# Kernel optimization log

Hardware: AMD Instinct MI355X
Metric: run time of the kernel (lower is better)

The kernel has to match this reference:

```python
import jax, jax.numpy as jnp
import numpy as np

SPARSE_SHAPE = (41, 1600, 1408)  # (D, H, W), batch_size = 1
N_VOXELS = 200000
BN_EPS = 1e-3


def _kernel_offsets():
    # 27 offsets of a 3x3x3 kernel, padding=1 -> offsets in {-1,0,1}^3
    g = np.stack(np.meshgrid(*([np.arange(-1, 2)] * 3), indexing='ij'), axis=-1)
    return jnp.asarray(g.reshape(-1, 3), dtype=jnp.int32)  # (27, 3)


def _neighbor_map(coords):
    """Submanifold rulebook: for each active voxel and each of 27 offsets,
    index of the active neighbor voxel, or N (sentinel) if inactive/out-of-bounds."""
    D, H, W = SPARSE_SHAPE
    N = coords.shape[0]
    b, z, y, x = coords[:, 0], coords[:, 1], coords[:, 2], coords[:, 3]
    flat = ((b * D + z) * H + y) * W + x  # batch_size=1
    grid = jnp.full((D * H * W,), N, dtype=jnp.int32).at[flat].set(
        jnp.arange(N, dtype=jnp.int32))
    offs = _kernel_offsets()                      # (27, 3)
    nc = coords[:, None, 1:4] + offs[None]        # (N, 27, 3)
    lim = jnp.asarray([D, H, W], dtype=jnp.int32)
    valid = jnp.all((nc >= 0) & (nc < lim), axis=-1)  # (N, 27)
    nflat = ((b[:, None] * D + nc[..., 0]) * H + nc[..., 1]) * W + nc[..., 2]
    nbr = jnp.where(valid, grid[jnp.where(valid, nflat, 0)], N)
    return nbr  # (N, 27) int32, sentinel = N


def _subm_conv(features, nbr, w):
    # gather -> batched small GEMM -> (implicit) scatter back to same voxels
    pad = jnp.concatenate(
        [features, jnp.zeros((1, features.shape[1]), features.dtype)], axis=0)
    gathered = pad[nbr]                           # (N, 27, Cin)
    return jnp.einsum('nkc,kcd->nd', gathered, w)  # (N, Cout)


def _bn_relu(x, gamma, beta):
    # BatchNorm1d in train mode over the voxel (batch) dim, eps=1e-3
    mean = x.mean(axis=0)
    var = x.var(axis=0)
    return jax.nn.relu((x - mean) * jax.lax.rsqrt(var + BN_EPS) * gamma + beta)


def setup_inputs() -> dict:
    D, H, W = SPARSE_SHAPE
    total = D * H * W
    rng = np.random.default_rng(0)
    # unique active voxel locations
    flat = np.unique(rng.integers(0, total, size=N_VOXELS + 20000))
    rng.shuffle(flat)
    flat = flat[:N_VOXELS]
    assert flat.shape[0] == N_VOXELS
    z = flat // (H * W)
    y = (flat // W) % H
    x = flat % W
    b = np.zeros_like(z)
    coords = jnp.asarray(np.stack([b, z, y, x], axis=1), dtype=jnp.int32)

    key = jax.random.key(0)
    k0, k1, k2 = jax.random.split(key, 3)
    features = jax.random.uniform(k0, (N_VOXELS, 3), dtype=jnp.float32)
    w1 = jax.random.normal(k1, (27, 3, 16), dtype=jnp.float32) * 0.1
    w2 = jax.random.normal(k2, (27, 16, 16), dtype=jnp.float32) * 0.05
    return {
        'features': features, 'coords': coords,
        'w1': w1, 'gamma1': jnp.ones(16, jnp.float32), 'beta1': jnp.zeros(16, jnp.float32),
        'w2': w2, 'gamma2': jnp.ones(16, jnp.float32), 'beta2': jnp.zeros(16, jnp.float32),
    }


def reference(features, coords, w1, gamma1, beta1, w2, gamma2, beta2):
    nbr = _neighbor_map(coords)   # shared indice_key='subm1' -> reused by both convs
    h = _bn_relu(_subm_conv(features, nbr, w1), gamma1, beta1)
    h = _bn_relu(_subm_conv(h, nbr, w2), gamma2, beta2)
    return h
```

## Files before the change

### kernel.cpp

```cpp
#include <hip/hip_runtime.h>
#include <stdint.h>

#define SPARSE_D 41
#define SPARSE_H 1600
#define SPARSE_W 1408
#define BN_EPS 0.001f

static constexpr int NYB = SPARSE_H / 2;
static constexpr int NBUCKET = SPARSE_D * NYB;
static constexpr int PCAP = 12;


__global__ void k_insert(const int* __restrict__ coords, uint32_t* __restrict__ bent, int N) {
    int n = blockIdx.x * blockDim.x + threadIdx.x;
    if (n >= N) return;
    int4 c4 = ((const int4*)coords)[n];
    int z = c4.y, y = c4.z, x = c4.w;
    int b = z * NYB + (y >> 1);
    uint32_t e = ((uint32_t)(y & 1) << 29) | ((uint32_t)x << 18) | (uint32_t)n;
    int slot = atomicAdd((int*)&bent[(size_t)b * 32], 1) + 1;
    if (slot <= 31) bent[(size_t)b * 32 + slot] = e;
}

__device__ __forceinline__ void stats_epilogue(const float acc[16],
                                               float* __restrict__ partials,
                                               float (*sred)[32]) {
    int lid = threadIdx.x & 63;
    int wid = threadIdx.x >> 6;
    #pragma unroll
    for (int d = 0; d < 16; ++d) {
        float v = acc[d];
        float v2 = v * v;
        #pragma unroll
        for (int off = 32; off; off >>= 1) {
            v += __shfl_xor(v, off);
            v2 += __shfl_xor(v2, off);
        }
        if (lid == 0) { sred[wid][d] = v; sred[wid][16 + d] = v2; }
    }
    __syncthreads();
    if (threadIdx.x < 32)
        partials[(size_t)blockIdx.x * 32 + threadIdx.x] =
            sred[0][threadIdx.x] + sred[1][threadIdx.x] +
            sred[2][threadIdx.x] + sred[3][threadIdx.x];
}

__global__ void k_build_conv1(const int* __restrict__ coords, const uint32_t* __restrict__ bent,
                              const float* __restrict__ feat, const float* __restrict__ w1,
                              int* __restrict__ pcnt, uint32_t* __restrict__ pairs,
                              float* __restrict__ h1, float* __restrict__ partials, int N) {
    __shared__ float sred[4][32];
    int n = blockIdx.x * blockDim.x + threadIdx.x;
    float acc[16];
    #pragma unroll
    for (int d = 0; d < 16; ++d) acc[d] = 0.f;
    if (n < N) {
        int4 c4 = ((const int4*)coords)[n];
        int z = c4.y, y = c4.z, x = c4.w;

        float f0 = feat[n * 3 + 0], f1 = feat[n * 3 + 1], f2 = feat[n * 3 + 2];
        const float* wd = w1 + 13 * 48;
        #pragma unroll
        for (int d = 0; d < 16; ++d)
            acc[d] = fmaf(f0, wd[d], fmaf(f1, wd[16 + d], f2 * wd[32 + d]));

        int yb0 = (y - 1) >> 1;
        uint4 q0[6];
        int bix[6], mm[6];
        #pragma unroll
        for (int p = 0; p < 6; ++p) {
            int zz = z + p / 2 - 1;
            int yb = yb0 + (p & 1);
            bool v = ((unsigned)zz < SPARSE_D) & ((unsigned)yb < NYB);
            int b = v ? (zz * NYB + yb) : 0;
            bix[p] = b;
            q0[p] = *(const uint4*)&bent[(size_t)b * 32];
            mm[p] = v ? 1 : 0;
        }

        uint32_t lpairs[PCAP];
        int cnt = 0;
        #pragma unroll
        for (int p = 0; p < 6; ++p) {
            int m = mm[p] ? min((int)q0[p].x, 31) : 0;
            int yb = yb0 + (p & 1);
            int dzk = (p / 2) * 9;
            auto scan_entry = [&](uint32_t e, int slot) {
                if (slot > m) return;
                int ey = (yb << 1) + (int)(e >> 29);
                int ex = (int)((e >> 18) & 0x7FFu);
                int dy = ey - y, dx = ex - x;
                if ((unsigned)(dy + 1) > 2u || (unsigned)(dx + 1) > 2u) return;
                uint32_t idx = e & 0x3FFFFu;
                if (idx == (uint32_t)n) return;
                int k = dzk + (dy + 1) * 3 + (dx + 1);
                if (cnt < PCAP) lpairs[cnt] = ((uint32_t)k << 18) | idx;
                ++cnt;
            };
            scan_entry(q0[p].y, 1);
            scan_entry(q0[p].z, 2);
            scan_entry(q0[p].w, 3);
            for (int w = 4; w <= m; w += 4) {
                uint4 q = *(const uint4*)&bent[(size_t)bix[p] * 32 + w];
                scan_entry(q.x, w);
                scan_entry(q.y, w + 1);
                scan_entry(q.z, w + 2);
                scan_entry(q.w, w + 3);
            }
        }
        cnt = min(cnt, PCAP);
        pcnt[n] = cnt;
        for (int c = 0; c < cnt; ++c) {
            uint32_t pr = lpairs[c];
            pairs[(size_t)c * N + n] = pr;
            int k = (int)(pr >> 18), idx = (int)(pr & 0x3FFFFu);
            float g0 = feat[idx * 3 + 0], g1 = feat[idx * 3 + 1], g2 = feat[idx * 3 + 2];
            const float* wk = w1 + k * 48;
            #pragma unroll
            for (int d = 0; d < 16; ++d)
                acc[d] = fmaf(g0, wk[d], fmaf(g1, wk[16 + d], fmaf(g2, wk[32 + d], acc[d])));
        }
        float4* o = (float4*)&h1[(size_t)n * 16];
        o[0] = make_float4(acc[0], acc[1], acc[2], acc[3]);
        o[1] = make_float4(acc[4], acc[5], acc[6], acc[7]);
        o[2] = make_float4(acc[8], acc[9], acc[10], acc[11]);
        o[3] = make_float4(acc[12], acc[13], acc[14], acc[15]);
    }
    stats_epilogue(acc, partials, sred);
}

__global__ void k_conv2(const float* __restrict__ h1, const int* __restrict__ pcnt,
                        const uint32_t* __restrict__ pairs, const float* __restrict__ w2,
                        const float* __restrict__ scsh1, float* __restrict__ out,
                        float* __restrict__ partials, int N) {
    __shared__ float sred[4][32];
    __shared__ float sc[16], sh[16];
    if (threadIdx.x < 16) { sc[threadIdx.x] = scsh1[threadIdx.x]; sh[threadIdx.x] = scsh1[16 + threadIdx.x]; }
    __syncthreads();
    int n = blockIdx.x * blockDim.x + threadIdx.x;
    float acc[16];
    #pragma unroll
    for (int d = 0; d < 16; ++d) acc[d] = 0.f;
    if (n < N) {
        float g[16];
        #pragma unroll
        for (int c = 0; c < 16; c += 4) {
            float4 t = *(const float4*)&h1[(size_t)n * 16 + c];
            g[c]     = fmaxf(fmaf(t.x, sc[c],     sh[c]),     0.f);
            g[c + 1] = fmaxf(fmaf(t.y, sc[c + 1], sh[c + 1]), 0.f);
            g[c + 2] = fmaxf(fmaf(t.z, sc[c + 2], sh[c + 2]), 0.f);
            g[c + 3] = fmaxf(fmaf(t.w, sc[c + 3], sh[c + 3]), 0.f);
        }
        {
            const float* w = w2 + 13 * 256;
            #pragma unroll
            for (int c = 0; c < 16; ++c)
                #pragma unroll
                for (int d = 0; d < 16; ++d)
                    acc[d] = fmaf(g[c], w[c * 16 + d], acc[d]);
        }
        int m = min(pcnt[n], PCAP);
        for (int cc = 0; cc < m; ++cc) {
            uint32_t pr = pairs[(size_t)cc * N + n];
            int k = (int)(pr >> 18), idx = (int)(pr & 0x3FFFFu);
            #pragma unroll
            for (int c = 0; c < 16; c += 4) {
                float4 t = *(const float4*)&h1[(size_t)idx * 16 + c];
                g[c]     = fmaxf(fmaf(t.x, sc[c],     sh[c]),     0.f);
                g[c + 1] = fmaxf(fmaf(t.y, sc[c + 1], sh[c + 1]), 0.f);
                g[c + 2] = fmaxf(fmaf(t.z, sc[c + 2], sh[c + 2]), 0.f);
                g[c + 3] = fmaxf(fmaf(t.w, sc[c + 3], sh[c + 3]), 0.f);
            }
            const float* wk = w2 + k * 256;
            #pragma unroll
            for (int c = 0; c < 16; ++c)
                #pragma unroll
                for (int d = 0; d < 16; ++d)
                    acc[d] = fmaf(g[c], wk[c * 16 + d], acc[d]);
        }
        float4* o = (float4*)&out[(size_t)n * 16];
        o[0] = make_float4(acc[0], acc[1], acc[2], acc[3]);
        o[1] = make_float4(acc[4], acc[5], acc[6], acc[7]);
        o[2] = make_float4(acc[8], acc[9], acc[10], acc[11]);
        o[3] = make_float4(acc[12], acc[13], acc[14], acc[15]);
    }
    stats_epilogue(acc, partials, sred);
}

__global__ void k_finalize(const float* __restrict__ partials, int nb,
                           const float* __restrict__ gamma, const float* __restrict__ beta,
                           float* __restrict__ scsh, float invN) {
    __shared__ float red[32][33];
    int ch = threadIdx.x & 31;
    int rg = threadIdx.x >> 5;
    float s0 = 0.f, s1 = 0.f, s2 = 0.f, s3 = 0.f;
    int j = rg;
    for (; j + 96 < nb; j += 128) {
        s0 += partials[(size_t)(j      ) * 32 + ch];
        s1 += partials[(size_t)(j + 32 ) * 32 + ch];
        s2 += partials[(size_t)(j + 64 ) * 32 + ch];
        s3 += partials[(size_t)(j + 96 ) * 32 + ch];
    }
    for (; j < nb; j += 32) s0 += partials[(size_t)j * 32 + ch];
    red[rg][ch] = (s0 + s1) + (s2 + s3);
    __syncthreads();
    if (threadIdx.x < 32) {
        float t = 0.f;
        #pragma unroll
        for (int r = 0; r < 32; ++r) t += red[r][threadIdx.x];
        red[0][threadIdx.x] = t;
    }
    __syncthreads();
    if (threadIdx.x < 16) {
        int d = threadIdx.x;
        float mean = red[0][d] * invN;
        float var = red[0][16 + d] * invN - mean * mean;
        float s2c = gamma[d] * rsqrtf(var + BN_EPS);
        scsh[d] = s2c;
        scsh[16 + d] = beta[d] - mean * s2c;
    }
}

__global__ void k_bnrelu4(float* __restrict__ x, const float* __restrict__ scsh, int nvec) {
    __shared__ float sc[16], sh[16];
    if (threadIdx.x < 16) { sc[threadIdx.x] = scsh[threadIdx.x]; sh[threadIdx.x] = scsh[16 + threadIdx.x]; }
    __syncthreads();
    int i = blockIdx.x * blockDim.x + threadIdx.x;
    if (i < nvec) {
        float4 v = ((float4*)x)[i];
        int c0 = (i & 3) * 4;
        v.x = fmaxf(fmaf(v.x, sc[c0 + 0], sh[c0 + 0]), 0.f);
        v.y = fmaxf(fmaf(v.y, sc[c0 + 1], sh[c0 + 1]), 0.f);
        v.z = fmaxf(fmaf(v.z, sc[c0 + 2], sh[c0 + 2]), 0.f);
        v.w = fmaxf(fmaf(v.w, sc[c0 + 3], sh[c0 + 3]), 0.f);
        ((float4*)x)[i] = v;
    }
}

extern "C" void kernel_launch(void* const* d_in, const int* in_sizes, int n_in,
                              void* d_out, int out_size, void* d_ws, size_t ws_size,
                              hipStream_t stream) {
    const float* feat   = (const float*)d_in[0];
    const int*   coords = (const int*)d_in[1];
    const float* w1     = (const float*)d_in[2];
    const float* gamma1 = (const float*)d_in[3];
    const float* beta1  = (const float*)d_in[4];
    const float* w2     = (const float*)d_in[5];
    const float* gamma2 = (const float*)d_in[6];
    const float* beta2  = (const float*)d_in[7];
    float* out = (float*)d_out;
    const int N = in_sizes[0] / 3;

    const int T = 256;
    const int nb = (N + T - 1) / T;
    const int nvec = N * 16 / 4;
    const int nbv = (nvec + T - 1) / T;

    char* ws = (char*)d_ws;
    size_t off = 0;
    uint32_t* bent = (uint32_t*)(ws + off);  off += (size_t)NBUCKET * 32 * 4;
    int* pcnt = (int*)(ws + off);            off += ((size_t)N * 4 + 63) & ~(size_t)63;
    uint32_t* pairs = (uint32_t*)(ws + off); off += (size_t)PCAP * N * 4;
    float* h1 = (float*)(ws + off);          off += (size_t)N * 16 * 4;
    float* partials = (float*)(ws + off);    off += ((size_t)nb * 32 * 4 + 63) & ~(size_t)63;
    float* stats = (float*)(ws + off);

    hipMemsetAsync(bent, 0, (size_t)NBUCKET * 32 * 4, stream);
    k_insert<<<nb, T, 0, stream>>>(coords, bent, N);
    k_build_conv1<<<nb, T, 0, stream>>>(coords, bent, feat, w1, pcnt, pairs, h1, partials, N);
    k_finalize<<<1, 1024, 0, stream>>>(partials, nb, gamma1, beta1, stats, 1.f / (float)N);
    k_conv2<<<nb, T, 0, stream>>>(h1, pcnt, pairs, w2, stats, out, partials, N);
    k_finalize<<<1, 1024, 0, stream>>>(partials, nb, gamma2, beta2, stats + 32, 1.f / (float)N);
    k_bnrelu4<<<nbv, T, 0, stream>>>(out, stats + 32, nvec);
}
```

Before: 152.9 us.

## Fuse all stages into one cooperative persistent kernel with grid syncs

Replaces the memset plus six kernel launches with a single cooperative persistent kernel. It zeroes the hash buckets, inserts voxels, builds the rulebook with conv1, reduces the BN stats, runs conv2 and the final BN+ReLU, using grid.sync between phases. Every block reduces the BN partials redundantly instead of relying on separate finalize kernels. This removes launch gaps and the single-block finalize kernels, but the grid is capped at occupancy (at most 1024 blocks) and adds several grid-wide barriers. The old multi-kernel path is kept as a fallback if cooperative launch fails. The fallback now uses fixed 1024-row partial buffers p1 and p2, which are smaller than the nb (about 782) times 32 floats it needs only if nb exceeds 1024.

Measured after the change: 547.7 us. 258% more time.

```diff
diff --git a/kernel.cpp b/kernel.cpp
--- a/kernel.cpp
+++ b/kernel.cpp
@@ -1,5 +1,8 @@
 #include <hip/hip_runtime.h>
+#include <hip/hip_cooperative_groups.h>
 #include <stdint.h>
+
+namespace cg = cooperative_groups;
 
 #define SPARSE_D 41
 #define SPARSE_H 1600
@@ -9,6 +12,255 @@
 static constexpr int NYB = SPARSE_H / 2;
 static constexpr int NBUCKET = SPARSE_D * NYB;
 static constexpr int PCAP = 12;
+
+
+
+__device__ __forceinline__ void acc_stats(const float acc[16], float (*smem)[33]) {
+    int lid = threadIdx.x & 63;
+    int wid = threadIdx.x >> 6;
+    #pragma unroll
+    for (int d = 0; d < 16; ++d) {
+        float v = acc[d];
+        float v2 = v * v;
+        #pragma unroll
+        for (int off = 32; off; off >>= 1) {
+            v  += __shfl_xor(v, off);
+            v2 += __shfl_xor(v2, off);
+        }
+        if (lid == 0) { smem[wid][d] += v; smem[wid][16 + d] += v2; }
+    }
+}
+
+__device__ __forceinline__ void block_finalize(const float* __restrict__ partials, int nbk,
+                                               const float* __restrict__ gamma,
+                                               const float* __restrict__ beta,
+                                               float invN, float (*smem)[33],
+                                               float* __restrict__ sc, float* __restrict__ sh) {
+    int ch = threadIdx.x & 31, rg = threadIdx.x >> 5;
+    float s0 = 0.f, s1 = 0.f, s2 = 0.f, s3 = 0.f;
+    int j = rg;
+    for (; j + 24 < nbk; j += 32) {
+        s0 += partials[(size_t)(j     ) * 32 + ch];
+        s1 += partials[(size_t)(j +  8) * 32 + ch];
+        s2 += partials[(size_t)(j + 16) * 32 + ch];
+        s3 += partials[(size_t)(j + 24) * 32 + ch];
+    }
+    for (; j < nbk; j += 8) s0 += partials[(size_t)j * 32 + ch];
+    __syncthreads();
+    smem[rg][ch] = (s0 + s1) + (s2 + s3);
+    __syncthreads();
+    if (threadIdx.x < 32) {
+        float t = 0.f;
+        #pragma unroll
+        for (int r = 0; r < 8; ++r) t += smem[r][threadIdx.x];
+        smem[0][threadIdx.x] = t;
+    }
+    __syncthreads();
+    if (threadIdx.x < 16) {
+        int d = threadIdx.x;
+        float mean = smem[0][d] * invN;
+        float var  = smem[0][16 + d] * invN - mean * mean;
+        float s2c  = gamma[d] * rsqrtf(var + BN_EPS);
+        sc[d] = s2c;
+        sh[d] = beta[d] - mean * s2c;
+    }
+    __syncthreads();
+}
+
+__global__ void __launch_bounds__(256, 2)
+k_fused(const float* __restrict__ feat, const int* __restrict__ coords,
+        const float* __restrict__ w1, const float* __restrict__ gamma1,
+        const float* __restrict__ beta1, const float* __restrict__ w2,
+        const float* __restrict__ gamma2, const float* __restrict__ beta2,
+        float* __restrict__ out, uint32_t* __restrict__ bent, int* __restrict__ pcnt,
+        uint32_t* __restrict__ pairs, float* __restrict__ h1,
+        float* __restrict__ p1, float* __restrict__ p2, int N, float invN) {
+    cg::grid_group grid = cg::this_grid();
+    __shared__ float smem[8][33];
+    __shared__ float sc[16], sh[16];
+    const int G   = (int)gridDim.x * 256;
+    const int tid = (int)blockIdx.x * 256 + (int)threadIdx.x;
+
+    for (int i = tid; i < NBUCKET * 8; i += G)
+        ((uint4*)bent)[i] = make_uint4(0u, 0u, 0u, 0u);
+    __threadfence();
+    grid.sync();
+
+    for (int n = tid; n < N; n += G) {
+        int4 c4 = ((const int4*)coords)[n];
+        int z = c4.y, y = c4.z, x = c4.w;
+        int b = z * NYB + (y >> 1);
+        uint32_t e = ((uint32_t)(y & 1) << 29) | ((uint32_t)x << 18) | (uint32_t)n;
+        int slot = atomicAdd((int*)&bent[(size_t)b * 32], 1) + 1;
+        if (slot <= 31) bent[(size_t)b * 32 + slot] = e;
+    }
+    __threadfence();
+    grid.sync();
+
+    for (int i = threadIdx.x; i < 8 * 33; i += 256) ((float*)smem)[i] = 0.f;
+    __syncthreads();
+    const int nit = (N + G - 1) / G;
+    for (int it = 0; it < nit; ++it) {
+        int n = tid + it * G;
+        float acc[16];
+        #pragma unroll
+        for (int d = 0; d < 16; ++d) acc[d] = 0.f;
+        if (n < N) {
+            int4 c4 = ((const int4*)coords)[n];
+            int z = c4.y, y = c4.z, x = c4.w;
+
+            float f0 = feat[n * 3 + 0], f1 = feat[n * 3 + 1], f2 = feat[n * 3 + 2];
+            const float* wd = w1 + 13 * 48;
+            #pragma unroll
+            for (int d = 0; d < 16; ++d)
+                acc[d] = fmaf(f0, wd[d], fmaf(f1, wd[16 + d], f2 * wd[32 + d]));
+
+            int yb0 = (y - 1) >> 1;
+            uint4 q0[6];
+            int bix[6], mm[6];
+            #pragma unroll
+            for (int p = 0; p < 6; ++p) {
+                int zz = z + p / 2 - 1;
+                int yb = yb0 + (p & 1);
+                bool v = ((unsigned)zz < SPARSE_D) & ((unsigned)yb < NYB);
+                int b = v ? (zz * NYB + yb) : 0;
+                bix[p] = b;
+                q0[p] = *(const uint4*)&bent[(size_t)b * 32];
+                mm[p] = v ? 1 : 0;
+            }
+
+            uint32_t lpairs[PCAP];
+            int cnt = 0;
+            #pragma unroll
+            for (int p = 0; p < 6; ++p) {
+                int m = mm[p] ? min((int)q0[p].x, 31) : 0;
+                int yb = yb0 + (p & 1);
+                int dzk = (p / 2) * 9;
+                auto scan_entry = [&](uint32_t e, int slot) {
+                    if (slot > m) return;
+                    int ey = (yb << 1) + (int)(e >> 29);
+                    int ex = (int)((e >> 18) & 0x7FFu);
+                    int dy = ey - y, dx = ex - x;
+                    if ((unsigned)(dy + 1) > 2u || (unsigned)(dx + 1) > 2u) return;
+                    uint32_t idx = e & 0x3FFFFu;
+                    if (idx == (uint32_t)n) return;
+                    int k = dzk + (dy + 1) * 3 + (dx + 1);
+                    if (cnt < PCAP) lpairs[cnt] = ((uint32_t)k << 18) | idx;
+                    ++cnt;
+                };
+                scan_entry(q0[p].y, 1);
+                scan_entry(q0[p].z, 2);
+                scan_entry(q0[p].w, 3);
+                for (int w = 4; w <= m; w += 4) {
+                    uint4 q = *(const uint4*)&bent[(size_t)bix[p] * 32 + w];
+                    scan_entry(q.x, w);
+                    scan_entry(q.y, w + 1);
+                    scan_entry(q.z, w + 2);
+                    scan_entry(q.w, w + 3);
+                }
+            }
+            cnt = min(cnt, PCAP);
+            pcnt[n] = cnt;
+            for (int c = 0; c < cnt; ++c) {
+                uint32_t pr = lpairs[c];
+                pairs[(size_t)c * N + n] = pr;
+                int k = (int)(pr >> 18), idx = (int)(pr & 0x3FFFFu);
+                float g0 = feat[idx * 3 + 0], g1 = feat[idx * 3 + 1], g2 = feat[idx * 3 + 2];
+                const float* wk = w1 + k * 48;
+                #pragma unroll
+                for (int d = 0; d < 16; ++d)
+                    acc[d] = fmaf(g0, wk[d], fmaf(g1, wk[16 + d], fmaf(g2, wk[32 + d], acc[d])));
+            }
+            float4* o = (float4*)&h1[(size_t)n * 16];
+            o[0] = make_float4(acc[0], acc[1], acc[2], acc[3]);
+            o[1] = make_float4(acc[4], acc[5], acc[6], acc[7]);
+            o[2] = make_float4(acc[8], acc[9], acc[10], acc[11]);
+            o[3] = make_float4(acc[12], acc[13], acc[14], acc[15]);
+        }
+        acc_stats(acc, smem);
+    }
+    __syncthreads();
+    if (threadIdx.x < 32)
+        p1[(size_t)blockIdx.x * 32 + threadIdx.x] =
+            smem[0][threadIdx.x] + smem[1][threadIdx.x] +
+            smem[2][threadIdx.x] + smem[3][threadIdx.x];
+    __threadfence();
+    grid.sync();
+
+    block_finalize(p1, (int)gridDim.x, gamma1, beta1, invN, smem, sc, sh);
+    __syncthreads();
+    for (int i = threadIdx.x; i < 8 * 33; i += 256) ((float*)smem)[i] = 0.f;
+    __syncthreads();
+
+    for (int it = 0; it < nit; ++it) {
+        int n = tid + it * G;
+        float acc[16];
+        #pragma unroll
+        for (int d = 0; d < 16; ++d) acc[d] = 0.f;
+        if (n < N) {
+            float g[16];
+            #pragma unroll
+            for (int c = 0; c < 16; c += 4) {
+                float4 t = *(const float4*)&h1[(size_t)n * 16 + c];
+                g[c]     = fmaxf(fmaf(t.x, sc[c],     sh[c]),     0.f);
+                g[c + 1] = fmaxf(fmaf(t.y, sc[c + 1], sh[c + 1]), 0.f);
+                g[c + 2] = fmaxf(fmaf(t.z, sc[c + 2], sh[c + 2]), 0.f);
+                g[c + 3] = fmaxf(fmaf(t.w, sc[c + 3], sh[c + 3]), 0.f);
+            }
+            {
+                const float* w = w2 + 13 * 256;
+                #pragma unroll
+                for (int c = 0; c < 16; ++c)
+                    #pragma unroll
+                    for (int d = 0; d < 16; ++d)
+                        acc[d] = fmaf(g[c], w[c * 16 + d], acc[d]);
+            }
+            int m = min(pcnt[n], PCAP);
+            for (int cc = 0; cc < m; ++cc) {
+                uint32_t pr = pairs[(size_t)cc * N + n];
+                int k = (int)(pr >> 18), idx = (int)(pr & 0x3FFFFu);
+                #pragma unroll
+                for (int c = 0; c < 16; c += 4) {
+                    float4 t = *(const float4*)&h1[(size_t)idx * 16 + c];
+                    g[c]     = fmaxf(fmaf(t.x, sc[c],     sh[c]),     0.f);
+                    g[c + 1] = fmaxf(fmaf(t.y, sc[c + 1], sh[c + 1]), 0.f);
+                    g[c + 2] = fmaxf(fmaf(t.z, sc[c + 2], sh[c + 2]), 0.f);
+                    g[c + 3] = fmaxf(fmaf(t.w, sc[c + 3], sh[c + 3]), 0.f);
+                }
+                const float* wk = w2 + k * 256;
+                #pragma unroll
+                for (int c = 0; c < 16; ++c)
+                    #pragma unroll
+                    for (int d = 0; d < 16; ++d)
+                        acc[d] = fmaf(g[c], wk[c * 16 + d], acc[d]);
+            }
+            float4* o = (float4*)&out[(size_t)n * 16];
+            o[0] = make_float4(acc[0], acc[1], acc[2], acc[3]);
+            o[1] = make_float4(acc[4], acc[5], acc[6], acc[7]);
+            o[2] = make_float4(acc[8], acc[9], acc[10], acc[11]);
+            o[3] = make_float4(acc[12], acc[13], acc[14], acc[15]);
+        }
+        acc_stats(acc, smem);
+    }
+    __syncthreads();
+    if (threadIdx.x < 32)
+        p2[(size_t)blockIdx.x * 32 + threadIdx.x] =
+            smem[0][threadIdx.x] + smem[1][threadIdx.x] +
+            smem[2][threadIdx.x] + smem[3][threadIdx.x];
+    __threadfence();
+    grid.sync();
+
+    block_finalize(p2, (int)gridDim.x, gamma2, beta2, invN, smem, sc, sh);
+    for (int i = tid; i < N * 4; i += G) {
+        float4 v = ((float4*)out)[i];
+        int c0 = (i & 3) * 4;
+        v.x = fmaxf(fmaf(v.x, sc[c0 + 0], sh[c0 + 0]), 0.f);
+        v.y = fmaxf(fmaf(v.y, sc[c0 + 1], sh[c0 + 1]), 0.f);
+        v.z = fmaxf(fmaf(v.z, sc[c0 + 2], sh[c0 + 2]), 0.f);
+        v.w = fmaxf(fmaf(v.w, sc[c0 + 3], sh[c0 + 3]), 0.f);
+        ((float4*)out)[i] = v;
+    }
+}
 
 
 __global__ void k_insert(const int* __restrict__ coords, uint32_t* __restrict__ bent, int N) {
@@ -57,13 +309,11 @@
     if (n < N) {
         int4 c4 = ((const int4*)coords)[n];
         int z = c4.y, y = c4.z, x = c4.w;
-
         float f0 = feat[n * 3 + 0], f1 = feat[n * 3 + 1], f2 = feat[n * 3 + 2];
         const float* wd = w1 + 13 * 48;
         #pragma unroll
         for (int d = 0; d < 16; ++d)
             acc[d] = fmaf(f0, wd[d], fmaf(f1, wd[16 + d], f2 * wd[32 + d]));
-
         int yb0 = (y - 1) >> 1;
         uint4 q0[6];
         int bix[6], mm[6];
@@ -77,7 +327,6 @@
             q0[p] = *(const uint4*)&bent[(size_t)b * 32];
             mm[p] = v ? 1 : 0;
         }
-
         uint32_t lpairs[PCAP];
         int cnt = 0;
         #pragma unroll
@@ -237,6 +486,7 @@
     }
 }
 
+
 extern "C" void kernel_launch(void* const* d_in, const int* in_sizes, int n_in,
                               void* d_out, int out_size, void* d_ws, size_t ws_size,
                               hipStream_t stream) {
@@ -262,14 +512,47 @@
     int* pcnt = (int*)(ws + off);            off += ((size_t)N * 4 + 63) & ~(size_t)63;
     uint32_t* pairs = (uint32_t*)(ws + off); off += (size_t)PCAP * N * 4;
     float* h1 = (float*)(ws + off);          off += (size_t)N * 16 * 4;
-    float* partials = (float*)(ws + off);    off += ((size_t)nb * 32 * 4 + 63) & ~(size_t)63;
+    float* p1 = (float*)(ws + off);          off += (size_t)1024 * 32 * 4;
+    float* p2 = (float*)(ws + off);          off += (size_t)1024 * 32 * 4;
     float* stats = (float*)(ws + off);
 
-    hipMemsetAsync(bent, 0, (size_t)NBUCKET * 32 * 4, stream);
-    k_insert<<<nb, T, 0, stream>>>(coords, bent, N);
-    k_build_conv1<<<nb, T, 0, stream>>>(coords, bent, feat, w1, pcnt, pairs, h1, partials, N);
-    k_finalize<<<1, 1024, 0, stream>>>(partials, nb, gamma1, beta1, stats, 1.f / (float)N);
-    k_conv2<<<nb, T, 0, stream>>>(h1, pcnt, pairs, w2, stats, out, partials, N);
-    k_finalize<<<1, 1024, 0, stream>>>(partials, nb, gamma2, beta2, stats + 32, 1.f / (float)N);
-    k_bnrelu4<<<nbv, T, 0, stream>>>(out, stats + 32, nvec);
-}
+    static int s_grid = 0;
+    static int s_coop = -1;
+    if (s_coop < 0) {
+        int dev = 0;
+        hipGetDevice(&dev);
+        int coop = 0;
+        hipDeviceGetAttribute(&coop, hipDeviceAttributeCooperativeLaunch, dev);
+        hipDeviceProp_t prop{};
+        hipGetDeviceProperties(&prop, dev);
+        int maxB = 0;
+        hipOccupancyMaxActiveBlocksPerMultiprocessor(&maxB, k_fused, T, 0);
+        s_grid = maxB * prop.multiProcessorCount;
+        if (s_grid > 1024) s_grid = 1024;
+        s_coop = (coop && s_grid >= 64) ? 1 : 0;
+    }
+
+    bool done = false;
+    if (s_coop == 1) {
+        int grid = s_grid < nb ? s_grid : nb;
+        float invN = 1.f / (float)N;
+        int Nv = N;
+        void* args[] = { (void*)&feat, (void*)&coords, (void*)&w1, (void*)&gamma1, (void*)&beta1,
+                         (void*)&w2, (void*)&gamma2, (void*)&beta2, (void*)&out,
+                         (void*)&bent, (void*)&pcnt, (void*)&pairs, (void*)&h1,
+                         (void*)&p1, (void*)&p2, (void*)&Nv, (void*)&invN };
+        hipError_t e = hipLaunchCooperativeKernel((const void*)k_fused, dim3(grid), dim3(T),
+                                                  args, 0, stream);
+        done = (e == hipSuccess);
+    }
+
+    if (!done) {
+        hipMemsetAsync(bent, 0, (size_t)NBUCKET * 32 * 4, stream);
+        k_insert<<<nb, T, 0, stream>>>(coords, bent, N);
+        k_build_conv1<<<nb, T, 0, stream>>>(coords, bent, feat, w1, pcnt, pairs, h1, p1, N);
+        k_finalize<<<1, 1024, 0, stream>>>(p1, nb, gamma1, beta1, stats, 1.f / (float)N);
+        k_conv2<<<nb, T, 0, stream>>>(h1, pcnt, pairs, w2, stats, out, p2, N);
+        k_finalize<<<1, 1024, 0, stream>>>(p2, nb, gamma2, beta2, stats + 32, 1.f / (float)N);
+        k_bnrelu4<<<nbv, T, 0, stream>>>(out, stats + 32, nvec);
+    }
+}
```

## Fuse BN stat finalization into conv kernels via last-block ticket

Applied to the files above, without the earlier changes.

Removes the two separate single-block finalize kernel launches. Each conv block now publishes its partial sums with a release store and takes a ticket from an atomic counter, and the last block to finish reduces all partials and writes the BN scale and shift. The counters sit next to the bucket table, so the existing memset clears them. This saves two launches and their gaps, but the final reduction now runs in one 256-thread block instead of 1024 threads, and the tail block does extra serial work.

After: 228.9 us. +49.7%, slower.

```diff
diff --git a/kernel.cpp b/kernel.cpp
--- a/kernel.cpp
+++ b/kernel.cpp
@@ -39,17 +39,58 @@
         if (lid == 0) { sred[wid][d] = v; sred[wid][16 + d] = v2; }
     }
     __syncthreads();
-    if (threadIdx.x < 32)
-        partials[(size_t)blockIdx.x * 32 + threadIdx.x] =
-            sred[0][threadIdx.x] + sred[1][threadIdx.x] +
-            sred[2][threadIdx.x] + sred[3][threadIdx.x];
+    if (threadIdx.x < 32) {
+        float v = sred[0][threadIdx.x] + sred[1][threadIdx.x] +
+                  sred[2][threadIdx.x] + sred[3][threadIdx.x];
+        __hip_atomic_store(&partials[(size_t)blockIdx.x * 32 + threadIdx.x], v,
+                           __ATOMIC_RELEASE, __HIP_MEMORY_SCOPE_AGENT);
+    }
+}
+
+__device__ __forceinline__ void final256(const float* __restrict__ partials, int nbk,
+                                         const float* __restrict__ gamma,
+                                         const float* __restrict__ beta,
+                                         float* __restrict__ scsh, float invN) {
+    __shared__ float red[8][33];
+    int ch = threadIdx.x & 31, rg = threadIdx.x >> 5;
+    float s0 = 0.f, s1 = 0.f, s2 = 0.f, s3 = 0.f;
+    int j = rg;
+    for (; j + 24 < nbk; j += 32) {
+        s0 += __hip_atomic_load(&partials[(size_t)(j     ) * 32 + ch], __ATOMIC_RELAXED, __HIP_MEMORY_SCOPE_AGENT);
+        s1 += __hip_atomic_load(&partials[(size_t)(j +  8) * 32 + ch], __ATOMIC_RELAXED, __HIP_MEMORY_SCOPE_AGENT);
+        s2 += __hip_atomic_load(&partials[(size_t)(j + 16) * 32 + ch], __ATOMIC_RELAXED, __HIP_MEMORY_SCOPE_AGENT);
+        s3 += __hip_atomic_load(&partials[(size_t)(j + 24) * 32 + ch], __ATOMIC_RELAXED, __HIP_MEMORY_SCOPE_AGENT);
+    }
+    for (; j < nbk; j += 8)
+        s0 += __hip_atomic_load(&partials[(size_t)j * 32 + ch], __ATOMIC_RELAXED, __HIP_MEMORY_SCOPE_AGENT);
+    red[rg][ch] = (s0 + s1) + (s2 + s3);
+    __syncthreads();
+    if (threadIdx.x < 32) {
+        float t = 0.f;
+        #pragma unroll
+        for (int r = 0; r < 8; ++r) t += red[r][threadIdx.x];
+        red[0][threadIdx.x] = t;
+    }
+    __syncthreads();
+    if (threadIdx.x < 16) {
+        int d = threadIdx.x;
+        float mean = red[0][d] * invN;
+        float var  = red[0][16 + d] * invN - mean * mean;
+        float s2c  = gamma[d] * rsqrtf(var + BN_EPS);
+        scsh[d] = s2c;
+        scsh[16 + d] = beta[d] - mean * s2c;
+    }
 }
 
 __global__ void k_build_conv1(const int* __restrict__ coords, const uint32_t* __restrict__ bent,
                               const float* __restrict__ feat, const float* __restrict__ w1,
                               int* __restrict__ pcnt, uint32_t* __restrict__ pairs,
-                              float* __restrict__ h1, float* __restrict__ partials, int N) {
+                              float* __restrict__ h1, float* __restrict__ partials,
+                              uint32_t* __restrict__ ticket,
+                              const float* __restrict__ gamma, const float* __restrict__ beta,
+                              float* __restrict__ scsh, float invN, int N) {
     __shared__ float sred[4][32];
+    __shared__ int s_last;
     int n = blockIdx.x * blockDim.x + threadIdx.x;
     float acc[16];
     #pragma unroll
@@ -127,14 +168,23 @@
         o[3] = make_float4(acc[12], acc[13], acc[14], acc[15]);
     }
     stats_epilogue(acc, partials, sred);
+    __syncthreads();
+    if (threadIdx.x == 0)
+        s_last = (__hip_atomic_fetch_add(ticket, 1u, __ATOMIC_ACQ_REL,
+                                         __HIP_MEMORY_SCOPE_AGENT) == (uint32_t)(gridDim.x - 1));
+    __syncthreads();
+    if (s_last) final256(partials, (int)gridDim.x, gamma, beta, scsh, invN);
 }
 
 __global__ void k_conv2(const float* __restrict__ h1, const int* __restrict__ pcnt,
                         const uint32_t* __restrict__ pairs, const float* __restrict__ w2,
                         const float* __restrict__ scsh1, float* __restrict__ out,
-                        float* __restrict__ partials, int N) {
+                        float* __restrict__ partials, uint32_t* __restrict__ ticket,
+                        const float* __restrict__ gamma, const float* __restrict__ beta,
+                        float* __restrict__ scsh2, float invN, int N) {
     __shared__ float sred[4][32];
     __shared__ float sc[16], sh[16];
+    __shared__ int s_last;
     if (threadIdx.x < 16) { sc[threadIdx.x] = scsh1[threadIdx.x]; sh[threadIdx.x] = scsh1[16 + threadIdx.x]; }
     __syncthreads();
     int n = blockIdx.x * blockDim.x + threadIdx.x;
@@ -185,40 +235,12 @@
         o[3] = make_float4(acc[12], acc[13], acc[14], acc[15]);
     }
     stats_epilogue(acc, partials, sred);
-}
-
-__global__ void k_finalize(const float* __restrict__ partials, int nb,
-                           const float* __restrict__ gamma, const float* __restrict__ beta,
-                           float* __restrict__ scsh, float invN) {
-    __shared__ float red[32][33];
-    int ch = threadIdx.x & 31;
-    int rg = threadIdx.x >> 5;
-    float s0 = 0.f, s1 = 0.f, s2 = 0.f, s3 = 0.f;
-    int j = rg;
-    for (; j + 96 < nb; j += 128) {
-        s0 += partials[(size_t)(j      ) * 32 + ch];
-        s1 += partials[(size_t)(j + 32 ) * 32 + ch];
-        s2 += partials[(size_t)(j + 64 ) * 32 + ch];
-        s3 += partials[(size_t)(j + 96 ) * 32 + ch];
-    }
-    for (; j < nb; j += 32) s0 += partials[(size_t)j * 32 + ch];
-    red[rg][ch] = (s0 + s1) + (s2 + s3);
-    __syncthreads();
-    if (threadIdx.x < 32) {
-        float t = 0.f;
-        #pragma unroll
-        for (int r = 0; r < 32; ++r) t += red[r][threadIdx.x];
-        red[0][threadIdx.x] = t;
-    }
-    __syncthreads();
-    if (threadIdx.x < 16) {
-        int d = threadIdx.x;
-        float mean = red[0][d] * invN;
-        float var = red[0][16 + d] * invN - mean * mean;
-        float s2c = gamma[d] * rsqrtf(var + BN_EPS);
-        scsh[d] = s2c;
-        scsh[16 + d] = beta[d] - mean * s2c;
-    }
+    __syncthreads();
+    if (threadIdx.x == 0)
+        s_last = (__hip_atomic_fetch_add(ticket, 1u, __ATOMIC_ACQ_REL,
+                                         __HIP_MEMORY_SCOPE_AGENT) == (uint32_t)(gridDim.x - 1));
+    __syncthreads();
+    if (s_last) final256(partials, (int)gridDim.x, gamma, beta, scsh2, invN);
 }
 
 __global__ void k_bnrelu4(float* __restrict__ x, const float* __restrict__ scsh, int nvec) {
@@ -255,21 +277,24 @@
     const int nb = (N + T - 1) / T;
     const int nvec = N * 16 / 4;
     const int nbv = (nvec + T - 1) / T;
+    const float invN = 1.f / (float)N;
 
     char* ws = (char*)d_ws;
     size_t off = 0;
     uint32_t* bent = (uint32_t*)(ws + off);  off += (size_t)NBUCKET * 32 * 4;
+    uint32_t* ctrl = (uint32_t*)(ws + off);  off += 64;
     int* pcnt = (int*)(ws + off);            off += ((size_t)N * 4 + 63) & ~(size_t)63;
     uint32_t* pairs = (uint32_t*)(ws + off); off += (size_t)PCAP * N * 4;
     float* h1 = (float*)(ws + off);          off += (size_t)N * 16 * 4;
-    float* partials = (float*)(ws + off);    off += ((size_t)nb * 32 * 4 + 63) & ~(size_t)63;
+    float* p1 = (float*)(ws + off);          off += ((size_t)nb * 32 * 4 + 63) & ~(size_t)63;
+    float* p2 = (float*)(ws + off);          off += ((size_t)nb * 32 * 4 + 63) & ~(size_t)63;
     float* stats = (float*)(ws + off);
 
-    hipMemsetAsync(bent, 0, (size_t)NBUCKET * 32 * 4, stream);
+    hipMemsetAsync(bent, 0, (size_t)NBUCKET * 32 * 4 + 64, stream);
     k_insert<<<nb, T, 0, stream>>>(coords, bent, N);
-    k_build_conv1<<<nb, T, 0, stream>>>(coords, bent, feat, w1, pcnt, pairs, h1, partials, N);
-    k_finalize<<<1, 1024, 0, stream>>>(partials, nb, gamma1, beta1, stats, 1.f / (float)N);
-    k_conv2<<<nb, T, 0, stream>>>(h1, pcnt, pairs, w2, stats, out, partials, N);
-    k_finalize<<<1, 1024, 0, stream>>>(partials, nb, gamma2, beta2, stats + 32, 1.f / (float)N);
+    k_build_conv1<<<nb, T, 0, stream>>>(coords, bent, feat, w1, pcnt, pairs, h1, p1,
+                                        ctrl + 0, gamma1, beta1, stats, invN, N);
+    k_conv2<<<nb, T, 0, stream>>>(h1, pcnt, pairs, w2, stats, out, p2,
+                                  ctrl + 1, gamma2, beta2, stats + 32, invN, N);
     k_bnrelu4<<<nbv, T, 0, stream>>>(out, stats + 32, nvec);
 }
```
